# Performance work log

Measured on AMD Instinct MI355X. Metric: run time of the kernel, lower is better.

Reference implementation:

```python
import jax, jax.numpy as jnp
import numpy as np

B = 131072
OBS = 64
H = 512
LAT = 512
DPC = 32  # dim_per_component -> 16 components of size 32
LN_EPS = 1e-6  # flax nn.LayerNorm default


def _variance_scaling_uniform(key, shape, scale=1.0):
    # variance_scaling(scale, 'fan_avg', 'uniform')
    fan_in, fan_out = shape[0], shape[1]
    fan_avg = (fan_in + fan_out) / 2.0
    limit = np.sqrt(3.0 * scale / fan_avg)
    return jax.random.uniform(key, shape, jnp.float32, -limit, limit)


def setup_inputs() -> dict:
    key = jax.random.key(0)
    ks = jax.random.split(key, 8)
    inp = {
        'observations': jax.random.normal(ks[0], (B, OBS), jnp.float32),
        'goals': jax.random.normal(ks[1], (B, OBS), jnp.float32),
        'W0': _variance_scaling_uniform(ks[2], (OBS, H)),
        'b0': jnp.zeros((H,), jnp.float32),
        'ln0_s': jnp.ones((H,), jnp.float32),
        'ln0_b': jnp.zeros((H,), jnp.float32),
        'W1': _variance_scaling_uniform(ks[3], (H, H)),
        'b1': jnp.zeros((H,), jnp.float32),
        'ln1_s': jnp.ones((H,), jnp.float32),
        'ln1_b': jnp.zeros((H,), jnp.float32),
        'W2': _variance_scaling_uniform(ks[4], (H, H)),
        'b2': jnp.zeros((H,), jnp.float32),
        'ln2_s': jnp.ones((H,), jnp.float32),
        'ln2_b': jnp.zeros((H,), jnp.float32),
        'W3': _variance_scaling_uniform(ks[5], (H, LAT)),
        'b3': jnp.zeros((LAT,), jnp.float32),
        'alpha': jnp.zeros((), jnp.float32),
    }
    return inp


def _layer_norm(x, scale, bias):
    m = x.mean(axis=-1, keepdims=True)
    v = ((x - m) ** 2).mean(axis=-1, keepdims=True)
    return (x - m) / jnp.sqrt(v + LN_EPS) * scale + bias


def _phi(x, W0, b0, ln0_s, ln0_b, W1, b1, ln1_s, ln1_b, W2, b2, ln2_s, ln2_b, W3, b3):
    # LayerNormMLP with activate_final=False: gelu+LN after every layer except last
    x = _layer_norm(jax.nn.gelu(x @ W0 + b0), ln0_s, ln0_b)
    x = _layer_norm(jax.nn.gelu(x @ W1 + b1), ln1_s, ln1_b)
    x = _layer_norm(jax.nn.gelu(x @ W2 + b2), ln2_s, ln2_b)
    return x @ W3 + b3


def _iqe(phi_s, phi_g, alpha):
    # reshape [B, LAT] -> [B, n_components, DPC]
    x = phi_s.reshape(*phi_s.shape[:-1], -1, DPC)
    y = phi_g.reshape(*phi_g.shape[:-1], -1, DPC)
    valid = x < y
    xy = jnp.concatenate(jnp.broadcast_arrays(x, y), axis=-1)  # [B, C, 2*DPC]
    ixy = jnp.argsort(xy, axis=-1)
    sxy = jnp.take_along_axis(xy, ixy, axis=-1)
    neg_inc = jnp.take_along_axis(valid, ixy % DPC, axis=-1) * jnp.where(ixy < DPC, -1, 1)
    neg_inp = jnp.cumsum(neg_inc, axis=-1)
    neg_f = -1.0 * (neg_inp < 0)
    neg_incf = jnp.concatenate([neg_f[..., :1], neg_f[..., 1:] - neg_f[..., :-1]], axis=-1)
    components = (sxy * neg_incf).sum(axis=-1)  # [B, C]
    a = jax.nn.sigmoid(alpha)
    return a * components.mean(axis=-1) + (1.0 - a) * components.max(axis=-1)


def reference(observations, goals, W0, b0, ln0_s, ln0_b, W1, b1, ln1_s, ln1_b,
              W2, b2, ln2_s, ln2_b, W3, b3, alpha):
    params = (W0, b0, ln0_s, ln0_b, W1, b1, ln1_s, ln1_b, W2, b2, ln2_s, ln2_b, W3, b3)
    phi_s = _phi(observations, *params)
    phi_g = _phi(goals, *params)
    return _iqe(phi_s, phi_g, alpha)
```

## Files before the change

kernel.cpp:

```cpp
#include <hip/hip_runtime.h>
#include <hip/hip_bf16.h>
#include <hip/hip_fp16.h>

typedef unsigned short u16;
typedef unsigned int u32;
typedef __attribute__((ext_vector_type(8))) _Float16 f16x8;
typedef __attribute__((ext_vector_type(4))) float f32x4;

#define ROWS 32
#define SSTR 520
#define RSTR 20
#define NEG_INF (-3.0e38f)

__device__ __forceinline__ float bf2f(u16 b) {
  union { u32 u; float f; } c; c.u = ((u32)b) << 16; return c.f;
}
__device__ __forceinline__ u16 f2bf(float f) {
  union { float f; u32 u; } c; c.f = f;
  u32 r = c.u + 0x7FFFu + ((c.u >> 16) & 1u);
  return (u16)(r >> 16);
}
__device__ __forceinline__ float gelu_tanh(float x) {
  float u = 0.7978845608028654f * (x + 0.044715f * x * x * x);
  float e = __expf(2.f * u);
  float t = 1.f - 2.f / (e + 1.f);
  return 0.5f * x * (1.f + t);
}
__device__ __forceinline__ float ldp(const void* p, int i, int f32) {
  return f32 ? ((const float*)p)[i] : bf2f(((const u16*)p)[i]);
}
__device__ __forceinline__ f16x8 load8(const void* base, long off, int f32) {
  f16x8 r;
  if (f32) {
    const float4* p = (const float4*)((const float*)base + off);
    float4 a = p[0], b = p[1];
    r[0] = (_Float16)a.x; r[1] = (_Float16)a.y; r[2] = (_Float16)a.z; r[3] = (_Float16)a.w;
    r[4] = (_Float16)b.x; r[5] = (_Float16)b.y; r[6] = (_Float16)b.z; r[7] = (_Float16)b.w;
  } else {
    const u16* p = (const u16*)base + off;
#pragma unroll
    for (int i = 0; i < 8; ++i) r[i] = (_Float16)bf2f(p[i]);
  }
  return r;
}

__global__ void detect_dtype(const u16* __restrict__ obs, int* flag) {
  int l = threadIdx.x;
  float v = fabsf(bf2f(obs[2 * l]));
  if (v != v) v = 1e30f;
#pragma unroll
  for (int m = 1; m <= 32; m <<= 1) v = fmaxf(v, __shfl_xor(v, m, 64));
  if (l == 0) *flag = (v > 1000.0f) ? 1 : 0;
}

__global__ void pack_frag(const void* __restrict__ src, u16* __restrict__ dst,
                          const int* __restrict__ flag, int total,
                          int fshift, int cishift, int tmask) {
  int id = blockIdx.x * 256 + threadIdx.x;
  if (id >= total) return;
  int j = id & 7;
  int lane = (id >> 3) & 63;
  int fi = id >> 9;
  int w = fi >> fshift;
  int rem = fi & ((1 << fshift) - 1);
  int ci = rem >> cishift;
  int t = rem & tmask;
  int q = lane >> 4, r = lane & 15;
  int ch = w * 64 + ci * 16 + r;
  int k = t * 32 + q * 8 + j;
  float v = ldp(src, k * 512 + ch, *flag);
  dst[id] = __half_as_ushort(__float2half(v));
}

__global__ __launch_bounds__(512, 4) void gciqe_main(
    const void* __restrict__ obs, const void* __restrict__ goals,
    const u16* __restrict__ wT0, const u16* __restrict__ wT1,
    const u16* __restrict__ wT2, const u16* __restrict__ wT3,
    const void* __restrict__ b0, const void* __restrict__ b1,
    const void* __restrict__ b2, const void* __restrict__ b3,
    const void* __restrict__ ls0, const void* __restrict__ lb0,
    const void* __restrict__ ls1, const void* __restrict__ lb1,
    const void* __restrict__ ls2, const void* __restrict__ lb2,
    const void* __restrict__ alphap, void* __restrict__ out,
    const int* __restrict__ flagp)
{
  __shared__ __align__(16) u16 slab[ROWS * SSTR];
  __shared__ __align__(16) float red[ROWS * RSTR];

  const int f32 = *flagp;
  const int tid = threadIdx.x;
  const int lane = tid & 63, w = tid >> 6;
  const int r = lane & 15, q = lane >> 4;
  const int i0 = blockIdx.x * 16;

  f32x4 acc[4][2];

#pragma unroll
  for (int ci = 0; ci < 4; ++ci) {
    acc[ci][0] = (f32x4){0.f, 0.f, 0.f, 0.f};
    acc[ci][1] = (f32x4){0.f, 0.f, 0.f, 0.f};
  }
  {
    f16x8 bf0[2][2];
#pragma unroll
    for (int nt = 0; nt < 2; ++nt) {
      int row = nt * 16 + r;
      const void* base = (row & 1) ? goals : obs;
      long ro = (long)(i0 + (row >> 1)) * 64;
#pragma unroll
      for (int u = 0; u < 2; ++u)
        bf0[nt][u] = load8(base, ro + u * 32 + q * 8, f32);
    }
    const u16* w0base = wT0 + w * 4096;
#pragma unroll
    for (int ci = 0; ci < 4; ++ci) {
#pragma unroll
      for (int u = 0; u < 2; ++u) {
        f16x8 af = *(const f16x8*)(w0base + (ci * 2 + u) * 512 + lane * 8);
        acc[ci][0] = __builtin_amdgcn_mfma_f32_16x16x32_f16(af, bf0[0][u], acc[ci][0], 0, 0, 0);
        acc[ci][1] = __builtin_amdgcn_mfma_f32_16x16x32_f16(af, bf0[1][u], acc[ci][1], 0, 0, 0);
      }
    }
  }

  for (int l = 0; l <= 3; ++l) {
    if (l > 0) {
      const u16* wp = (l == 1) ? wT1 : (l == 2) ? wT2 : wT3;
      const u16* wbase = wp + w * 32768;
#pragma unroll
      for (int ci = 0; ci < 4; ++ci) {
        acc[ci][0] = (f32x4){0.f, 0.f, 0.f, 0.f};
        acc[ci][1] = (f32x4){0.f, 0.f, 0.f, 0.f};
      }
      f16x8 A[2][4];
#pragma unroll
      for (int u = 0; u < 4; ++u)
        A[0][u] = *(const f16x8*)(wbase + u * 512 + lane * 8);
#pragma unroll
      for (int kq = 0; kq < 4; ++kq) {
        f16x8 bfr[2][4];
#pragma unroll
        for (int nt = 0; nt < 2; ++nt)
#pragma unroll
          for (int u = 0; u < 4; ++u)
            bfr[nt][u] = *(const f16x8*)(slab + (nt * 16 + r) * SSTR + kq * 128 + u * 32 + q * 8);
#pragma unroll
        for (int ci = 0; ci < 4; ++ci) {
          const int step = kq * 4 + ci;
          const int cur = step & 1;
          if (step < 15) {
            const int nstep = step + 1;
            const int nci = nstep & 3, nkq = nstep >> 2;
#pragma unroll
            for (int u = 0; u < 4; ++u)
              A[cur ^ 1][u] = *(const f16x8*)(wbase + (nci * 16 + nkq * 4 + u) * 512 + lane * 8);
          }
#pragma unroll
          for (int u = 0; u < 4; ++u) {
            acc[ci][0] = __builtin_amdgcn_mfma_f32_16x16x32_f16(A[cur][u], bfr[0][u], acc[ci][0], 0, 0, 0);
            acc[ci][1] = __builtin_amdgcn_mfma_f32_16x16x32_f16(A[cur][u], bfr[1][u], acc[ci][1], 0, 0, 0);
          }
        }
      }
    }

    if (l < 3) {
      const void* pb  = (l == 0) ? b0 : (l == 1) ? b1 : b2;
      const void* psl = (l == 0) ? ls0 : (l == 1) ? ls1 : ls2;
      const void* plb = (l == 0) ? lb0 : (l == 1) ? lb1 : lb2;
      float bz[4][4];
#pragma unroll
      for (int ci = 0; ci < 4; ++ci) {
        int cb = w * 64 + ci * 16 + q * 4;
#pragma unroll
        for (int j = 0; j < 4; ++j) bz[ci][j] = ldp(pb, cb + j, f32);
      }
      float s[2] = {0.f, 0.f}, t[2] = {0.f, 0.f};
#pragma unroll
      for (int ci = 0; ci < 4; ++ci)
#pragma unroll
        for (int nt = 0; nt < 2; ++nt) {
          f32x4 v = acc[ci][nt];
          v.x = gelu_tanh(v.x + bz[ci][0]); v.y = gelu_tanh(v.y + bz[ci][1]);
          v.z = gelu_tanh(v.z + bz[ci][2]); v.w = gelu_tanh(v.w + bz[ci][3]);
          acc[ci][nt] = v;
          s[nt] += v.x + v.y + v.z + v.w;
          t[nt] += v.x * v.x + v.y * v.y + v.z * v.z + v.w * v.w;
        }
#pragma unroll
      for (int nt = 0; nt < 2; ++nt) {
        s[nt] += __shfl_xor(s[nt], 16, 64); t[nt] += __shfl_xor(t[nt], 16, 64);
        s[nt] += __shfl_xor(s[nt], 32, 64); t[nt] += __shfl_xor(t[nt], 32, 64);
      }
      if (q == 0) {
        *(float2*)(red + (0 * 16 + r) * RSTR + w * 2) = make_float2(s[0], t[0]);
        *(float2*)(red + (1 * 16 + r) * RSTR + w * 2) = make_float2(s[1], t[1]);
      }
      __syncthreads();
      float mean[2], rstd[2];
#pragma unroll
      for (int nt = 0; nt < 2; ++nt) {
        int row = nt * 16 + r;
        float ts = 0.f, tq = 0.f;
#pragma unroll
        for (int p = 0; p < 4; ++p) {
          f32x4 a = *(const f32x4*)(red + row * RSTR + p * 4);
          ts += a.x + a.z; tq += a.y + a.w;
        }
        mean[nt] = ts * (1.f / 512.f);
        rstd[nt] = rsqrtf(tq * (1.f / 512.f) - mean[nt] * mean[nt] + 1e-6f);
      }
      float gs[4][4], gb[4][4];
#pragma unroll
      for (int ci = 0; ci < 4; ++ci) {
        int cb = w * 64 + ci * 16 + q * 4;
#pragma unroll
        for (int j = 0; j < 4; ++j) {
          gs[ci][j] = ldp(psl, cb + j, f32);
          gb[ci][j] = ldp(plb, cb + j, f32);
        }
      }
#pragma unroll
      for (int ci = 0; ci < 4; ++ci) {
        int cb = w * 64 + ci * 16 + q * 4;
#pragma unroll
        for (int nt = 0; nt < 2; ++nt) {
          int row = nt * 16 + r;
          f32x4 v = acc[ci][nt];
          ushort4 o;
          o.x = __half_as_ushort(__float2half((v.x - mean[nt]) * rstd[nt] * gs[ci][0] + gb[ci][0]));
          o.y = __half_as_ushort(__float2half((v.y - mean[nt]) * rstd[nt] * gs[ci][1] + gb[ci][1]));
          o.z = __half_as_ushort(__float2half((v.z - mean[nt]) * rstd[nt] * gs[ci][2] + gb[ci][2]));
          o.w = __half_as_ushort(__float2half((v.w - mean[nt]) * rstd[nt] * gs[ci][3] + gb[ci][3]));
          *(ushort4*)(slab + row * SSTR + cb) = o;
        }
      }
      __syncthreads();
    } else {
#pragma unroll
      for (int ci = 0; ci < 4; ++ci) {
        int cb = w * 64 + ci * 16 + q * 4;
        float bx = ldp(b3, cb + 0, f32), by = ldp(b3, cb + 1, f32);
        float bz2 = ldp(b3, cb + 2, f32), bw = ldp(b3, cb + 3, f32);
#pragma unroll
        for (int nt = 0; nt < 2; ++nt) {
          int row = nt * 16 + r;
          f32x4 v = acc[ci][nt];
          ushort4 o;
          o.x = __half_as_ushort(__float2half(v.x + bx));
          o.y = __half_as_ushort(__float2half(v.y + by));
          o.z = __half_as_ushort(__float2half(v.z + bz2));
          o.w = __half_as_ushort(__float2half(v.w + bw));
          *(ushort4*)(slab + row * SSTR + cb) = o;
        }
      }
      __syncthreads();
    }
  }

  {
    const float al = ldp(alphap, 0, f32);
    const float a = 1.f / (1.f + __expf(-al));
    const int h = lane >> 5, il = lane & 31;
    for (int v = 0; v < 2; ++v) {
      int pL = 2 * w + v;
      float cs = 0.f, cm = 0.f;
      for (int it = 0; it < 8; ++it) {
        int c = 2 * it + h;
        float x = __half2float(__ushort_as_half(slab[(2 * pL) * SSTR + c * 32 + il]));
        float y = __half2float(__ushort_as_half(slab[(2 * pL + 1) * SSTR + c * 32 + il]));
        if (!(x < y)) y = NEG_INF;
#pragma unroll
        for (int k = 2; k <= 32; k <<= 1) {
#pragma unroll
          for (int j = k >> 1; j >= 1; j >>= 1) {
            float xo = __shfl_xor(x, j, 64);
            float yo = __shfl_xor(y, j, 64);
            bool keep_min = (((il & k) == 0) == ((il & j) == 0));
            bool take = keep_min ? (xo < x) : (xo > x);
            if (take) { x = xo; y = yo; }
          }
        }
        float p = __shfl_up(y, 1, 32);
        if (il == 0) p = NEG_INF;
#pragma unroll
        for (int d = 1; d <= 16; d <<= 1) {
          float t2 = __shfl_up(p, d, 32);
          if (il >= d) p = fmaxf(p, t2);
        }
        float contrib = fmaxf(0.f, y - fmaxf(x, p));
#pragma unroll
        for (int msk = 1; msk <= 16; msk <<= 1)
          contrib += __shfl_xor(contrib, msk, 64);
        cs += contrib;
        cm = fmaxf(cm, contrib);
      }
      cs += __shfl_xor(cs, 32, 64);
      cm = fmaxf(cm, __shfl_xor(cm, 32, 64));
      if (lane == 0) {
        float res = a * (cs * (1.f / 16.f)) + (1.f - a) * cm;
        if (f32) ((float*)out)[i0 + pL] = res;
        else ((u16*)out)[i0 + pL] = f2bf(res);
      }
    }
  }
}

extern "C" void kernel_launch(void* const* d_in, const int* in_sizes, int n_in,
                              void* d_out, int out_size, void* d_ws, size_t ws_size,
                              hipStream_t stream) {
  (void)in_sizes; (void)n_in; (void)out_size; (void)ws_size;
  const void* obs   = d_in[0];
  const void* goals = d_in[1];
  const void* W0 = d_in[2];
  const void* b0 = d_in[3];
  const void* ls0 = d_in[4];
  const void* lb0 = d_in[5];
  const void* W1 = d_in[6];
  const void* b1 = d_in[7];
  const void* ls1 = d_in[8];
  const void* lb1 = d_in[9];
  const void* W2 = d_in[10];
  const void* b2 = d_in[11];
  const void* ls2 = d_in[12];
  const void* lb2 = d_in[13];
  const void* W3 = d_in[14];
  const void* b3 = d_in[15];
  const void* alpha = d_in[16];

  int* flag = (int*)d_ws;
  u16* wT0 = (u16*)((char*)d_ws + 64);
  u16* wT1 = wT0 + 512 * 64;
  u16* wT2 = wT1 + 512 * 512;
  u16* wT3 = wT2 + 512 * 512;

  detect_dtype<<<1, 64, 0, stream>>>((const u16*)obs, flag);
  pack_frag<<<128, 256, 0, stream>>>(W0, wT0, flag, 512 * 64, 3, 1, 1);
  pack_frag<<<1024, 256, 0, stream>>>(W1, wT1, flag, 512 * 512, 6, 4, 15);
  pack_frag<<<1024, 256, 0, stream>>>(W2, wT2, flag, 512 * 512, 6, 4, 15);
  pack_frag<<<1024, 256, 0, stream>>>(W3, wT3, flag, 512 * 512, 6, 4, 15);
  gciqe_main<<<8192, 512, 0, stream>>>(obs, goals, wT0, wT1, wT2, wT3,
      b0, b1, b2, b3, ls0, lb0, ls1, lb1, ls2, lb2, alpha, d_out, flag);
}
```

Measured before the change: 1.137 ms.

## Double rows per block, fragment-ordered activation slab, cheaper GELU and integer-key sort

Each block now handles 32 pairs (64 rows) rather than 16, so every weight fragment loaded from global memory feeds four MFMA column tiles instead of two, halving weight traffic per row. The activation slab is stored in MFMA fragment order, so B operands are read as contiguous 16-byte loads without padding, and weight prefetch uses a three-slot ring. GELU is rewritten as x*sigmoid form with a hardware reciprocal, and the IQE bitonic sort packs encoded half keys and values into one u32, halving shuffles. In exchange the block uses about 64KB of LDS plus more accumulator registers, which lowers occupancy.

```diff
diff --git a/kernel.cpp b/kernel.cpp
--- a/kernel.cpp
+++ b/kernel.cpp
@@ -7,10 +7,7 @@
 typedef __attribute__((ext_vector_type(8))) _Float16 f16x8;
 typedef __attribute__((ext_vector_type(4))) float f32x4;
 
-#define ROWS 32
-#define SSTR 520
 #define RSTR 20
-#define NEG_INF (-3.0e38f)
 
 __device__ __forceinline__ float bf2f(u16 b) {
   union { u32 u; float f; } c; c.u = ((u32)b) << 16; return c.f;
@@ -21,10 +18,10 @@
   return (u16)(r >> 16);
 }
 __device__ __forceinline__ float gelu_tanh(float x) {
-  float u = 0.7978845608028654f * (x + 0.044715f * x * x * x);
-  float e = __expf(2.f * u);
-  float t = 1.f - 2.f / (e + 1.f);
-  return 0.5f * x * (1.f + t);
+  float x2 = x * x;
+  float t = __builtin_fmaf(0.044715f, x2, 1.0f);
+  float e = __expf(-1.5957691216057308f * (x * t));
+  return x * __builtin_amdgcn_rcpf(1.f + e);
 }
 __device__ __forceinline__ float ldp(const void* p, int i, int f32) {
   return f32 ? ((const float*)p)[i] : bf2f(((const u16*)p)[i]);
@@ -43,6 +40,15 @@
   }
   return r;
 }
+__device__ __forceinline__ u32 encH(u32 h) {
+  return (h & 0x8000u) ? (h ^ 0xFFFFu) : (h | 0x8000u);
+}
+__device__ __forceinline__ float decE(u32 e) {
+  u32 h = (e & 0x8000u) ? (e & 0x7FFFu) : (~e & 0xFFFFu);
+  return __half2float(__ushort_as_half((u16)h));
+}
+__device__ __forceinline__ u32 umin32(u32 a, u32 b) { return a < b ? a : b; }
+__device__ __forceinline__ u32 umax32(u32 a, u32 b) { return a > b ? a : b; }
 
 __global__ void detect_dtype(const u16* __restrict__ obs, int* flag) {
   int l = threadIdx.x;
@@ -76,34 +82,34 @@
     const void* __restrict__ obs, const void* __restrict__ goals,
     const u16* __restrict__ wT0, const u16* __restrict__ wT1,
     const u16* __restrict__ wT2, const u16* __restrict__ wT3,
-    const void* __restrict__ b0, const void* __restrict__ b1,
-    const void* __restrict__ b2, const void* __restrict__ b3,
+    const void* __restrict__ b0p, const void* __restrict__ b1p,
+    const void* __restrict__ b2p, const void* __restrict__ b3p,
     const void* __restrict__ ls0, const void* __restrict__ lb0,
     const void* __restrict__ ls1, const void* __restrict__ lb1,
     const void* __restrict__ ls2, const void* __restrict__ lb2,
     const void* __restrict__ alphap, void* __restrict__ out,
     const int* __restrict__ flagp)
 {
-  __shared__ __align__(16) u16 slab[ROWS * SSTR];
-  __shared__ __align__(16) float red[ROWS * RSTR];
+  __shared__ __align__(16) u16 slab[64 * 512];
+  __shared__ __align__(16) float red[64 * RSTR];
 
   const int f32 = *flagp;
   const int tid = threadIdx.x;
   const int lane = tid & 63, w = tid >> 6;
   const int r = lane & 15, q = lane >> 4;
-  const int i0 = blockIdx.x * 16;
-
-  f32x4 acc[4][2];
-
-#pragma unroll
-  for (int ci = 0; ci < 4; ++ci) {
-    acc[ci][0] = (f32x4){0.f, 0.f, 0.f, 0.f};
-    acc[ci][1] = (f32x4){0.f, 0.f, 0.f, 0.f};
-  }
+  const int i0 = blockIdx.x * 32;
+
+  f32x4 acc[4][4];
+
+#pragma unroll
+  for (int ci = 0; ci < 4; ++ci)
+#pragma unroll
+    for (int nt = 0; nt < 4; ++nt)
+      acc[ci][nt] = (f32x4){0.f, 0.f, 0.f, 0.f};
   {
-    f16x8 bf0[2][2];
-#pragma unroll
-    for (int nt = 0; nt < 2; ++nt) {
+    f16x8 bf0[4][2];
+#pragma unroll
+    for (int nt = 0; nt < 4; ++nt) {
       int row = nt * 16 + r;
       const void* base = (row & 1) ? goals : obs;
       long ro = (long)(i0 + (row >> 1)) * 64;
@@ -113,14 +119,14 @@
     }
     const u16* w0base = wT0 + w * 4096;
 #pragma unroll
-    for (int ci = 0; ci < 4; ++ci) {
+    for (int ci = 0; ci < 4; ++ci)
 #pragma unroll
       for (int u = 0; u < 2; ++u) {
         f16x8 af = *(const f16x8*)(w0base + (ci * 2 + u) * 512 + lane * 8);
-        acc[ci][0] = __builtin_amdgcn_mfma_f32_16x16x32_f16(af, bf0[0][u], acc[ci][0], 0, 0, 0);
-        acc[ci][1] = __builtin_amdgcn_mfma_f32_16x16x32_f16(af, bf0[1][u], acc[ci][1], 0, 0, 0);
-      }
-    }
+#pragma unroll
+        for (int nt = 0; nt < 4; ++nt)
+          acc[ci][nt] = __builtin_amdgcn_mfma_f32_16x16x32_f16(af, bf0[nt][u], acc[ci][nt], 0, 0, 0);
+      }
   }
 
   for (int l = 0; l <= 3; ++l) {
@@ -128,78 +134,72 @@
       const u16* wp = (l == 1) ? wT1 : (l == 2) ? wT2 : wT3;
       const u16* wbase = wp + w * 32768;
 #pragma unroll
-      for (int ci = 0; ci < 4; ++ci) {
-        acc[ci][0] = (f32x4){0.f, 0.f, 0.f, 0.f};
-        acc[ci][1] = (f32x4){0.f, 0.f, 0.f, 0.f};
-      }
-      f16x8 A[2][4];
-#pragma unroll
-      for (int u = 0; u < 4; ++u)
-        A[0][u] = *(const f16x8*)(wbase + u * 512 + lane * 8);
-#pragma unroll
-      for (int kq = 0; kq < 4; ++kq) {
-        f16x8 bfr[2][4];
-#pragma unroll
-        for (int nt = 0; nt < 2; ++nt)
-#pragma unroll
-          for (int u = 0; u < 4; ++u)
-            bfr[nt][u] = *(const f16x8*)(slab + (nt * 16 + r) * SSTR + kq * 128 + u * 32 + q * 8);
-#pragma unroll
-        for (int ci = 0; ci < 4; ++ci) {
-          const int step = kq * 4 + ci;
-          const int cur = step & 1;
-          if (step < 15) {
-            const int nstep = step + 1;
-            const int nci = nstep & 3, nkq = nstep >> 2;
-#pragma unroll
-            for (int u = 0; u < 4; ++u)
-              A[cur ^ 1][u] = *(const f16x8*)(wbase + (nci * 16 + nkq * 4 + u) * 512 + lane * 8);
+      for (int ci = 0; ci < 4; ++ci)
+#pragma unroll
+        for (int nt = 0; nt < 4; ++nt)
+          acc[ci][nt] = (f32x4){0.f, 0.f, 0.f, 0.f};
+      f16x8 A[3];
+      A[0] = *(const f16x8*)(wbase + lane * 8);
+      A[1] = *(const f16x8*)(wbase + 16 * 512 + lane * 8);
+#pragma unroll
+      for (int kq = 0; kq < 4; ++kq)
+#pragma unroll
+        for (int u = 0; u < 4; ++u) {
+          f16x8 B0 = *(const f16x8*)(slab + (0 * 16 + kq * 4 + u) * 512 + lane * 8);
+          f16x8 B1 = *(const f16x8*)(slab + (1 * 16 + kq * 4 + u) * 512 + lane * 8);
+          f16x8 B2 = *(const f16x8*)(slab + (2 * 16 + kq * 4 + u) * 512 + lane * 8);
+          f16x8 B3 = *(const f16x8*)(slab + (3 * 16 + kq * 4 + u) * 512 + lane * 8);
+#pragma unroll
+          for (int ci = 0; ci < 4; ++ci) {
+            const int s = kq * 16 + u * 4 + ci;
+            if (s + 2 < 64) {
+              const int s2 = s + 2;
+              const int nci = s2 & 3, nu = (s2 >> 2) & 3, nkq = s2 >> 4;
+              A[s2 % 3] = *(const f16x8*)(wbase + (nci * 16 + nkq * 4 + nu) * 512 + lane * 8);
+            }
+            const f16x8 af = A[s % 3];
+            acc[ci][0] = __builtin_amdgcn_mfma_f32_16x16x32_f16(af, B0, acc[ci][0], 0, 0, 0);
+            acc[ci][1] = __builtin_amdgcn_mfma_f32_16x16x32_f16(af, B1, acc[ci][1], 0, 0, 0);
+            acc[ci][2] = __builtin_amdgcn_mfma_f32_16x16x32_f16(af, B2, acc[ci][2], 0, 0, 0);
+            acc[ci][3] = __builtin_amdgcn_mfma_f32_16x16x32_f16(af, B3, acc[ci][3], 0, 0, 0);
           }
-#pragma unroll
-          for (int u = 0; u < 4; ++u) {
-            acc[ci][0] = __builtin_amdgcn_mfma_f32_16x16x32_f16(A[cur][u], bfr[0][u], acc[ci][0], 0, 0, 0);
-            acc[ci][1] = __builtin_amdgcn_mfma_f32_16x16x32_f16(A[cur][u], bfr[1][u], acc[ci][1], 0, 0, 0);
-          }
-        }
-      }
+        }
     }
 
     if (l < 3) {
-      const void* pb  = (l == 0) ? b0 : (l == 1) ? b1 : b2;
+      const void* pb  = (l == 0) ? b0p : (l == 1) ? b1p : b2p;
       const void* psl = (l == 0) ? ls0 : (l == 1) ? ls1 : ls2;
       const void* plb = (l == 0) ? lb0 : (l == 1) ? lb1 : lb2;
-      float bz[4][4];
+      float s_[4] = {0.f, 0.f, 0.f, 0.f}, t_[4] = {0.f, 0.f, 0.f, 0.f};
 #pragma unroll
       for (int ci = 0; ci < 4; ++ci) {
         int cb = w * 64 + ci * 16 + q * 4;
-#pragma unroll
-        for (int j = 0; j < 4; ++j) bz[ci][j] = ldp(pb, cb + j, f32);
-      }
-      float s[2] = {0.f, 0.f}, t[2] = {0.f, 0.f};
-#pragma unroll
-      for (int ci = 0; ci < 4; ++ci)
-#pragma unroll
-        for (int nt = 0; nt < 2; ++nt) {
+        float bx = ldp(pb, cb + 0, f32), by = ldp(pb, cb + 1, f32);
+        float bz = ldp(pb, cb + 2, f32), bw = ldp(pb, cb + 3, f32);
+#pragma unroll
+        for (int nt = 0; nt < 4; ++nt) {
           f32x4 v = acc[ci][nt];
-          v.x = gelu_tanh(v.x + bz[ci][0]); v.y = gelu_tanh(v.y + bz[ci][1]);
-          v.z = gelu_tanh(v.z + bz[ci][2]); v.w = gelu_tanh(v.w + bz[ci][3]);
+          v.x = gelu_tanh(v.x + bx); v.y = gelu_tanh(v.y + by);
+          v.z = gelu_tanh(v.z + bz); v.w = gelu_tanh(v.w + bw);
           acc[ci][nt] = v;
-          s[nt] += v.x + v.y + v.z + v.w;
-          t[nt] += v.x * v.x + v.y * v.y + v.z * v.z + v.w * v.w;
-        }
-#pragma unroll
-      for (int nt = 0; nt < 2; ++nt) {
-        s[nt] += __shfl_xor(s[nt], 16, 64); t[nt] += __shfl_xor(t[nt], 16, 64);
-        s[nt] += __shfl_xor(s[nt], 32, 64); t[nt] += __shfl_xor(t[nt], 32, 64);
+          s_[nt] += v.x + v.y + v.z + v.w;
+          t_[nt] += v.x * v.x + v.y * v.y + v.z * v.z + v.w * v.w;
+        }
+      }
+#pragma unroll
+      for (int nt = 0; nt < 4; ++nt) {
+        s_[nt] += __shfl_xor(s_[nt], 16, 64); t_[nt] += __shfl_xor(t_[nt], 16, 64);
+        s_[nt] += __shfl_xor(s_[nt], 32, 64); t_[nt] += __shfl_xor(t_[nt], 32, 64);
       }
       if (q == 0) {
-        *(float2*)(red + (0 * 16 + r) * RSTR + w * 2) = make_float2(s[0], t[0]);
-        *(float2*)(red + (1 * 16 + r) * RSTR + w * 2) = make_float2(s[1], t[1]);
+#pragma unroll
+        for (int nt = 0; nt < 4; ++nt)
+          *(float2*)(red + (nt * 16 + r) * RSTR + w * 2) = make_float2(s_[nt], t_[nt]);
       }
       __syncthreads();
-      float mean[2], rstd[2];
-#pragma unroll
-      for (int nt = 0; nt < 2; ++nt) {
+      float mean[4], rstd[4];
+#pragma unroll
+      for (int nt = 0; nt < 4; ++nt) {
         int row = nt * 16 + r;
         float ts = 0.f, tq = 0.f;
 #pragma unroll
@@ -210,48 +210,44 @@
         mean[nt] = ts * (1.f / 512.f);
         rstd[nt] = rsqrtf(tq * (1.f / 512.f) - mean[nt] * mean[nt] + 1e-6f);
       }
-      float gs[4][4], gb[4][4];
 #pragma unroll
       for (int ci = 0; ci < 4; ++ci) {
         int cb = w * 64 + ci * 16 + q * 4;
-#pragma unroll
-        for (int j = 0; j < 4; ++j) {
-          gs[ci][j] = ldp(psl, cb + j, f32);
-          gb[ci][j] = ldp(plb, cb + j, f32);
-        }
-      }
+        float g0 = ldp(psl, cb + 0, f32), g1 = ldp(psl, cb + 1, f32);
+        float g2 = ldp(psl, cb + 2, f32), g3 = ldp(psl, cb + 3, f32);
+        float h0 = ldp(plb, cb + 0, f32), h1 = ldp(plb, cb + 1, f32);
+        float h2 = ldp(plb, cb + 2, f32), h3 = ldp(plb, cb + 3, f32);
+        int fragk = ((cb >> 7) << 2) + ((cb >> 5) & 3);
+        int sub = ((cb >> 3) & 3) * 128 + r * 8 + (cb & 7);
+#pragma unroll
+        for (int nt = 0; nt < 4; ++nt) {
+          f32x4 v = acc[ci][nt];
+          ushort4 o;
+          o.x = __half_as_ushort(__float2half((v.x - mean[nt]) * rstd[nt] * g0 + h0));
+          o.y = __half_as_ushort(__float2half((v.y - mean[nt]) * rstd[nt] * g1 + h1));
+          o.z = __half_as_ushort(__float2half((v.z - mean[nt]) * rstd[nt] * g2 + h2));
+          o.w = __half_as_ushort(__float2half((v.w - mean[nt]) * rstd[nt] * g3 + h3));
+          *(ushort4*)(slab + (nt * 16 + fragk) * 512 + sub) = o;
+        }
+      }
+      __syncthreads();
+    } else {
+      __syncthreads();
 #pragma unroll
       for (int ci = 0; ci < 4; ++ci) {
         int cb = w * 64 + ci * 16 + q * 4;
-#pragma unroll
-        for (int nt = 0; nt < 2; ++nt) {
-          int row = nt * 16 + r;
-          f32x4 v = acc[ci][nt];
-          ushort4 o;
-          o.x = __half_as_ushort(__float2half((v.x - mean[nt]) * rstd[nt] * gs[ci][0] + gb[ci][0]));
-          o.y = __half_as_ushort(__float2half((v.y - mean[nt]) * rstd[nt] * gs[ci][1] + gb[ci][1]));
-          o.z = __half_as_ushort(__float2half((v.z - mean[nt]) * rstd[nt] * gs[ci][2] + gb[ci][2]));
-          o.w = __half_as_ushort(__float2half((v.w - mean[nt]) * rstd[nt] * gs[ci][3] + gb[ci][3]));
-          *(ushort4*)(slab + row * SSTR + cb) = o;
-        }
-      }
-      __syncthreads();
-    } else {
-#pragma unroll
-      for (int ci = 0; ci < 4; ++ci) {
-        int cb = w * 64 + ci * 16 + q * 4;
-        float bx = ldp(b3, cb + 0, f32), by = ldp(b3, cb + 1, f32);
-        float bz2 = ldp(b3, cb + 2, f32), bw = ldp(b3, cb + 3, f32);
-#pragma unroll
-        for (int nt = 0; nt < 2; ++nt) {
+        float bx = ldp(b3p, cb + 0, f32), by = ldp(b3p, cb + 1, f32);
+        float bz = ldp(b3p, cb + 2, f32), bw = ldp(b3p, cb + 3, f32);
+#pragma unroll
+        for (int nt = 0; nt < 4; ++nt) {
           int row = nt * 16 + r;
           f32x4 v = acc[ci][nt];
           ushort4 o;
           o.x = __half_as_ushort(__float2half(v.x + bx));
           o.y = __half_as_ushort(__float2half(v.y + by));
-          o.z = __half_as_ushort(__float2half(v.z + bz2));
+          o.z = __half_as_ushort(__float2half(v.z + bz));
           o.w = __half_as_ushort(__float2half(v.w + bw));
-          *(ushort4*)(slab + row * SSTR + cb) = o;
+          *(ushort4*)(slab + row * 512 + cb) = o;
         }
       }
       __syncthreads();
@@ -260,35 +256,35 @@
 
   {
     const float al = ldp(alphap, 0, f32);
-    const float a = 1.f / (1.f + __expf(-al));
+    const float aa = 1.f / (1.f + __expf(-al));
     const int h = lane >> 5, il = lane & 31;
-    for (int v = 0; v < 2; ++v) {
-      int pL = 2 * w + v;
+    for (int pv = 0; pv < 4; ++pv) {
+      int pL = 4 * w + pv;
       float cs = 0.f, cm = 0.f;
       for (int it = 0; it < 8; ++it) {
         int c = 2 * it + h;
-        float x = __half2float(__ushort_as_half(slab[(2 * pL) * SSTR + c * 32 + il]));
-        float y = __half2float(__ushort_as_half(slab[(2 * pL + 1) * SSTR + c * 32 + il]));
-        if (!(x < y)) y = NEG_INF;
-#pragma unroll
-        for (int k = 2; k <= 32; k <<= 1) {
+        u32 xh = slab[(2 * pL) * 512 + c * 32 + il];
+        u32 yh = slab[(2 * pL + 1) * 512 + c * 32 + il];
+        u32 ex = encH(xh), ey = encH(yh);
+        u32 sv = (ex << 16) | ((ex < ey) ? ey : 0x03FFu);
+#pragma unroll
+        for (int k = 2; k <= 32; k <<= 1)
 #pragma unroll
           for (int j = k >> 1; j >= 1; j >>= 1) {
-            float xo = __shfl_xor(x, j, 64);
-            float yo = __shfl_xor(y, j, 64);
-            bool keep_min = (((il & k) == 0) == ((il & j) == 0));
-            bool take = keep_min ? (xo < x) : (xo > x);
-            if (take) { x = xo; y = yo; }
+            u32 so = __shfl_xor(sv, j, 64);
+            u32 mn = umin32(sv, so), mx = umax32(sv, so);
+            bool up = ((il & k) == 0) == ((il & j) == 0);
+            sv = up ? mn : mx;
           }
-        }
-        float p = __shfl_up(y, 1, 32);
-        if (il == 0) p = NEG_INF;
+        u32 ye = sv & 0xFFFFu;
+        u32 p = __shfl_up(ye, 1, 32);
+        if (il == 0) p = 0u;
 #pragma unroll
         for (int d = 1; d <= 16; d <<= 1) {
-          float t2 = __shfl_up(p, d, 32);
-          if (il >= d) p = fmaxf(p, t2);
-        }
-        float contrib = fmaxf(0.f, y - fmaxf(x, p));
+          u32 t2 = __shfl_up(p, d, 32);
+          if (il >= d) p = umax32(p, t2);
+        }
+        float contrib = fmaxf(0.f, decE(ye) - decE(umax32(sv >> 16, p)));
 #pragma unroll
         for (int msk = 1; msk <= 16; msk <<= 1)
           contrib += __shfl_xor(contrib, msk, 64);
@@ -298,7 +294,7 @@
       cs += __shfl_xor(cs, 32, 64);
       cm = fmaxf(cm, __shfl_xor(cm, 32, 64));
       if (lane == 0) {
-        float res = a * (cs * (1.f / 16.f)) + (1.f - a) * cm;
+        float res = aa * (cs * (1.f / 16.f)) + (1.f - aa) * cm;
         if (f32) ((float*)out)[i0 + pL] = res;
         else ((u16*)out)[i0 + pL] = f2bf(res);
       }
@@ -339,6 +335,6 @@
   pack_frag<<<1024, 256, 0, stream>>>(W1, wT1, flag, 512 * 512, 6, 4, 15);
   pack_frag<<<1024, 256, 0, stream>>>(W2, wT2, flag, 512 * 512, 6, 4, 15);
   pack_frag<<<1024, 256, 0, stream>>>(W3, wT3, flag, 512 * 512, 6, 4, 15);
-  gciqe_main<<<8192, 512, 0, stream>>>(obs, goals, wT0, wT1, wT2, wT3,
+  gciqe_main<<<4096, 512, 0, stream>>>(obs, goals, wT0, wT1, wT2, wT3,
       b0, b1, b2, b3, ls0, lb0, ls1, lb1, ls2, lb2, alpha, d_out, flag);
 }
```

Result: slower. 1.174 ms (+3.2%).
